# Kernel optimization log

Measured on AMD Instinct MI355X. Metric: run time of the kernel, lower is better.

Reference implementation:

```python
import jax, jax.numpy as jnp
import numpy as np

S, N, CIN, H, W = 8, 32, 128, 16, 16
COUT, K = 128, 3
F = CIN * K * K          # in_features = Cin*k*k = 1152
LAM = float(F)           # NealPrior: var = 1/fan_in -> precision = fan_in


def extract_patches(x):
    # x: [S,N,Cin,H,W] -> [S,N,F,H*W] patches, torch-unfold ordering (Cin outer, then ki,kj)
    p = K // 2
    xp = jnp.pad(x, ((0, 0), (0, 0), (0, 0), (p, p), (p, p)))
    pats = jnp.stack([xp[..., i:i + H, j:j + W] for i in range(K) for j in range(K)], axis=3)
    # pats: [S,N,Cin,K*K,H,W]
    return pats.reshape(x.shape[0], x.shape[1], F, H * W)


def setup_inputs() -> dict:
    key = jax.random.key(0)
    k1, k2, k3, k4 = jax.random.split(key, 4)
    X = jax.random.normal(k1, (S, N, CIN, H, W), jnp.float32)
    u = jax.random.normal(k2, (N, COUT, H, W), jnp.float32)
    log_prec_scaled = -4.0 + 0.1 * jax.random.normal(k3, (N,), jnp.float32)
    Z = jax.random.normal(k4, (S, F, COUT), jnp.float32)  # reparam noise (t.randn in torch fwd)
    return {"X": X, "u": u, "log_prec_scaled": log_prec_scaled, "Z": Z}


def reference(X, u, log_prec_scaled, Z):
    # sqrt per-inducing-point precision (log_prec_lr = 1.0)
    sqrt_prec = jnp.exp(0.5 * log_prec_scaled)
    Xil = sqrt_prec[None, :, None, None, None] * X       # [S,N,Cin,H,W]
    Yil = sqrt_prec[:, None, None, None] * u             # [N,Cout,H,W]

    Xu = extract_patches(Xil)                            # [S,N,F,L]
    Yr = Yil.reshape(N, COUT, H * W)                     # [N,Cout,L]

    XLX = jnp.einsum('snfl,sngl->sfg', Xu, Xu)           # [S,F,F]
    XLY = jnp.einsum('snfl,ncl->sfc', Xu, Yr)            # [S,F,Cout]

    prec = XLX + LAM * jnp.eye(F, dtype=X.dtype)         # add isotropic Neal prior precision
    L = jnp.linalg.cholesky(prec)                        # [S,F,F]
    logdet = 2.0 * jnp.sum(jnp.log(jnp.diagonal(L, axis1=-2, axis2=-1)), -1)  # [S]
    logdet_total = COUT * logdet                         # expand over out_features then sum

    # posterior mean: prec^{-1} XLY via two triangular solves (cholesky_solve)
    t1 = jax.scipy.linalg.solve_triangular(L, XLY, lower=True)
    mu = jax.scipy.linalg.solve_triangular(L, t1, lower=True, trans=1)
    # dW solves L^T dW = Z (triangular_solve upper=False, transpose=True)
    dW = jax.scipy.linalg.solve_triangular(L, Z, lower=True, trans=1)

    sample_fc = mu + dW                                  # [S,F,Cout]
    sample = jnp.swapaxes(sample_fc, -1, -2)             # [S,Cout,F] (torch layout)

    # logP: unnormalized MVN log-prob under isotropic Neal prior precision LAM
    logP = -0.5 * LAM * jnp.sum(sample_fc ** 2, (-1, -2)) \
           + 0.5 * COUT * F * jnp.log(jnp.asarray(LAM, X.dtype))
    logQ = -0.5 * jnp.sum(Z ** 2, (-1, -2)) + 0.5 * logdet_total
    logpq = logP - logQ                                  # [S]
    return sample, logpq
```

## Files before the change

### kernel.cpp

```cpp
#include <hip/hip_runtime.h>
#include <hip/hip_bf16.h>
#include <math.h>

#define NS    8
#define NNI   32
#define NCI   128
#define NHH   16
#define NWW   16
#define NCO   128
#define NFF   1152
#define NLL   256
#define LAMV  1152.0f
#define COOPG 512

typedef short s8v __attribute__((ext_vector_type(8)));
typedef float f4v __attribute__((ext_vector_type(4)));

#define AS1 __attribute__((address_space(1)))
#define AS3 __attribute__((address_space(3)))

__device__ __forceinline__ float rdl(float v, int l) {
  return __uint_as_float(__builtin_amdgcn_readlane(__float_as_uint(v), (unsigned)l));
}

#define WAVE_LDS_FENCE() asm volatile("s_waitcnt lgkmcnt(0)" ::: "memory")

__global__ __launch_bounds__(256) void k_build_Xu(const float* __restrict__ X,
                                                  const float* __restrict__ lp,
                                                  unsigned short* __restrict__ Xu,
                                                  int nz) {
  unsigned idx = blockIdx.x * 256u + threadIdx.x;
  unsigned m = idx & 8191u;
  unsigned f = idx >> 13;
  unsigned n = m >> 8, l = m & 255u, h = l >> 4, w = l & 15u;
  unsigned c = f / 9u, a = f - 9u * c;
  unsigned ki = a / 3u, kj = a - 3u * ki;
  int hi = (int)(h + ki) - 1, wi = (int)(w + kj) - 1;
  bool inb = (hi >= 0 && hi < NHH && wi >= 0 && wi < NWW);
  size_t xoff = (((size_t)n * NCI + c) << 8) + (size_t)(unsigned)(hi * NWW + wi);
  float spn = expf(0.5f * lp[n]);
  for (int z = 0; z < nz; ++z) {
    float v = inb ? X[(size_t)z * 1048576 + xoff] : 0.f;
    __hip_bfloat16 hv = __float2bfloat16(spn * v);
    Xu[(size_t)z * (NFF * 8192) + idx] = *(unsigned short*)&hv;
  }
}

__global__ __launch_bounds__(256) void k_build_B(const float* __restrict__ u,
                                                 const float* __restrict__ lp,
                                                 unsigned short* __restrict__ Bm) {
  unsigned idx = blockIdx.x * 256u + threadIdx.x;
  unsigned m = idx & 8191u;
  unsigned c = idx >> 13;
  unsigned n = m >> 8, l = m & 255u;
  float spn = expf(0.5f * lp[n]);
  __hip_bfloat16 hv = __float2bfloat16(spn * u[((size_t)n * NCO + c) * NLL + l]);
  Bm[idx] = *(unsigned short*)&hv;
}

__global__ void k_diag_init(float* __restrict__ prec) {
  int s = blockIdx.y;
  int i = blockIdx.x * 256 + threadIdx.x;
  if (i < NFF) prec[(size_t)s * NFF * NFF + (size_t)i * NFF + i] = LAMV;
}

__global__ __launch_bounds__(256) void k_mfma(const unsigned short* __restrict__ XuBase,
                                              const unsigned short* __restrict__ Bm,
                                              float* __restrict__ prec,
                                              float* __restrict__ XLY,
                                              int kLen, int direct) {
  __shared__ unsigned short As[8192];
  __shared__ unsigned short Bs[8192];
  int z = blockIdx.z;
  const unsigned short* Xu = XuBase + (size_t)z * (NFF * 8192);
  prec += (size_t)z * NFF * NFF;
  XLY += (size_t)z * NFF * NCO;
  int bx = blockIdx.x;
  int row0, col0;
  const unsigned short* Ag;
  const unsigned short* Bg;
  bool isXLX;
  if (bx < 45) {
    int b = 0;
    while ((b + 1) * (b + 2) / 2 <= bx) b++;
    row0 = b * 128;
    col0 = (bx - b * (b + 1) / 2) * 128;
    Bg = Xu + (size_t)col0 * 8192;
    isXLX = true;
  } else {
    row0 = (bx - 45) * 128;
    col0 = 0;
    Bg = Bm;
    isXLX = false;
  }
  Ag = Xu + (size_t)row0 * 8192;

  int t = threadIdx.x;
  int lane = t & 63, w = t >> 6;
  int wm = w & 1, wn = w >> 1;
  int n16 = lane & 15, q = lane >> 4;
  int srow = lane >> 3, sch = lane & 7;

  f4v acc[4][4];
#pragma unroll
  for (int i = 0; i < 4; ++i)
#pragma unroll
    for (int j = 0; j < 4; ++j) acc[i][j] = (f4v)0.f;

  int kBase = blockIdx.y * kLen;
  for (int k0 = kBase; k0 < kBase + kLen; k0 += 64) {
    __syncthreads();
#pragma unroll
    for (int it = 0; it < 4; ++it) {
      int rA = (w * 4 + it) * 8 + srow;
      int cA = (sch - rA) & 7;
      const unsigned short* gpa = Ag + (size_t)rA * 8192 + k0 + cA * 8;
      const unsigned short* gpb = Bg + (size_t)rA * 8192 + k0 + cA * 8;
      __builtin_amdgcn_global_load_lds((AS1 const void*)gpa,
                                       (AS3 void*)&As[(w * 4 + it) * 512], 16, 0, 0);
      __builtin_amdgcn_global_load_lds((AS1 const void*)gpb,
                                       (AS3 void*)&Bs[(w * 4 + it) * 512], 16, 0, 0);
    }
    __syncthreads();
#pragma unroll
    for (int kk = 0; kk < 2; ++kk) {
      s8v af[4], bf[4];
#pragma unroll
      for (int im = 0; im < 4; ++im) {
        int r = wm * 64 + im * 16 + n16;
        int slot = ((kk * 4 + q) + r) & 7;
        af[im] = *(const s8v*)&As[r * 64 + slot * 8];
      }
#pragma unroll
      for (int in = 0; in < 4; ++in) {
        int r = wn * 64 + in * 16 + n16;
        int slot = ((kk * 4 + q) + r) & 7;
        bf[in] = *(const s8v*)&Bs[r * 64 + slot * 8];
      }
#pragma unroll
      for (int im = 0; im < 4; ++im)
#pragma unroll
        for (int in = 0; in < 4; ++in)
          acc[im][in] = __builtin_amdgcn_mfma_f32_16x16x32_bf16(af[im], bf[in], acc[im][in], 0, 0, 0);
    }
  }

#pragma unroll
  for (int im = 0; im < 4; ++im)
#pragma unroll
    for (int in = 0; in < 4; ++in) {
      int gr = row0 + wm * 64 + im * 16 + q * 4;
      int gc = (isXLX ? col0 : 0) + wn * 64 + in * 16 + n16;
      if (direct) {
        if (isXLX) {
#pragma unroll
          for (int tt = 0; tt < 4; ++tt)
            prec[(size_t)(gr + tt) * NFF + gc] =
                acc[im][in][tt] + ((gr + tt) == gc ? LAMV : 0.f);
        } else {
#pragma unroll
          for (int tt = 0; tt < 4; ++tt)
            XLY[(size_t)(gr + tt) * NCO + gc] = acc[im][in][tt];
        }
      } else {
        if (isXLX) {
#pragma unroll
          for (int tt = 0; tt < 4; ++tt)
            atomicAdd(&prec[(size_t)(gr + tt) * NFF + gc], acc[im][in][tt]);
        } else {
#pragma unroll
          for (int tt = 0; tt < 4; ++tt)
            atomicAdd(&XLY[(size_t)(gr + tt) * NCO + gc], acc[im][in][tt]);
        }
      }
    }
}

__device__ __forceinline__ void xsync(unsigned* slot, unsigned* go, unsigned role,
                                      unsigned cnt, unsigned ep) {
  __syncthreads();
  int t = threadIdx.x;
  if (t == 0)
    __hip_atomic_store(&slot[role], ep, __ATOMIC_RELAXED, __HIP_MEMORY_SCOPE_AGENT);
  if (role == 0) {
    if (t < 64) {
      for (;;) {
        unsigned ok = 1;
        for (unsigned i = (unsigned)t; i < cnt; i += 64u)
          ok &= (__hip_atomic_load(&slot[i], __ATOMIC_RELAXED, __HIP_MEMORY_SCOPE_AGENT) >= ep)
                    ? 1u : 0u;
        if (__all((int)ok)) break;
        __builtin_amdgcn_s_sleep(2);
      }
      if (t == 0)
        __hip_atomic_store(go, ep, __ATOMIC_RELAXED, __HIP_MEMORY_SCOPE_AGENT);
    }
  } else if (t == 0) {
    while (__hip_atomic_load(go, __ATOMIC_RELAXED, __HIP_MEMORY_SCOPE_AGENT) < ep)
      __builtin_amdgcn_s_sleep(2);
  }
  __syncthreads();
  asm volatile("buffer_inv" ::: "memory");
  __syncthreads();
}

__device__ void dev_fact64(float* D, float* accum_ld, int lane) {
  float x[64];
#pragma unroll
  for (int k = 0; k < 64; ++k) x[k] = D[(size_t)lane * NFF + k];
  float ld = 0.f;
#pragma unroll
  for (int k = 0; k < 64; ++k) {
    float dk = sqrtf(rdl(x[k], k));
    float inv = 1.0f / dk;
    ld += logf(dk);
    x[k] = (lane == k) ? dk : ((lane > k) ? x[k] * inv : x[k]);
#pragma unroll
    for (int kk = k + 1; kk < 64; ++kk)
      x[kk] = fmaf(-x[k], rdl(x[k], kk), x[kk]);
  }
  if (lane == 0) atomicAdd(accum_ld, 2.f * ld);
#pragma unroll
  for (int k = 0; k < 64; ++k) D[(size_t)lane * NFF + k] = x[k];
}

__device__ void dev_panel(float* Ps, int p, int i, float* smw) {
  float (*Xs)[66] = (float(*)[66])smw;
  const float* Dp = Ps + (size_t)(p * 64) * NFF + p * 64;
  float* Ai = Ps + (size_t)(i * 64) * NFF + p * 64;
  float* At = Ps + (size_t)(p * 64) * NFF + i * 64;
  int lane = threadIdx.x & 63;
  float Lc[64];
#pragma unroll
  for (int k = 0; k < 64; ++k) Lc[k] = Dp[(size_t)k * NFF + lane];
  for (int r = 0; r < 64; ++r) Xs[r][lane] = Ai[(size_t)r * NFF + lane];
  WAVE_LDS_FENCE();
  float x[64];
#pragma unroll
  for (int k = 0; k < 64; ++k) x[k] = Xs[lane][k];
#pragma unroll
  for (int j = 0; j < 64; ++j) {
    float xj = x[j] / rdl(Lc[j], j);
    x[j] = xj;
#pragma unroll
    for (int k = j + 1; k < 64; ++k)
      x[k] = fmaf(-xj, rdl(Lc[k], j), x[k]);
  }
#pragma unroll
  for (int k = 0; k < 64; ++k) Xs[lane][k] = x[k];
  WAVE_LDS_FENCE();
  for (int r = 0; r < 64; ++r) At[(size_t)r * NFF + lane] = Xs[lane][r];
}

__device__ void dev_trail(float* Ps, float* accum, int p, int idx, float* sm) {
  int b = 0;
  while ((b + 1) * (b + 2) / 2 <= idx) b++;
  int c = idx - b * (b + 1) / 2;
  int i = p + 1 + b, j = p + 1 + c;
  const float* Ui = Ps + (size_t)(p * 64) * NFF + i * 64;
  const float* Uj = Ps + (size_t)(p * 64) * NFF + j * 64;
  float* Cb = Ps + (size_t)(i * 64) * NFF + j * 64;
  float (*Ak)[68] = (float(*)[68])sm;
  float (*Bk)[68] = (float(*)[68])(sm + 4352);
  int t = threadIdx.x, tx = t & 15, ty = t >> 4;
  __syncthreads();
  for (int e = t; e < 1024; e += 256) {
    int k = e >> 4, c4 = (e & 15) * 4;
    *(float4*)&Ak[k][c4] = *(const float4*)(Ui + (size_t)k * NFF + c4);
    *(float4*)&Bk[k][c4] = *(const float4*)(Uj + (size_t)k * NFF + c4);
  }
  __syncthreads();
  float acc[4][4];
#pragma unroll
  for (int a = 0; a < 4; ++a)
#pragma unroll
    for (int b2 = 0; b2 < 4; ++b2) acc[a][b2] = 0.f;
#pragma unroll
  for (int kk = 0; kk < 64; ++kk) {
    float av[4], bv[4];
    *(float4*)&av[0] = *(const float4*)&Ak[kk][ty * 4];
    *(float4*)&bv[0] = *(const float4*)&Bk[kk][tx * 4];
#pragma unroll
    for (int a = 0; a < 4; ++a)
#pragma unroll
      for (int b2 = 0; b2 < 4; ++b2) acc[a][b2] = fmaf(av[a], bv[b2], acc[a][b2]);
  }
  if (!(b == 0 && c == 0)) {
#pragma unroll
    for (int a = 0; a < 4; ++a) {
      float4* cp = (float4*)(Cb + (size_t)(ty * 4 + a) * NFF + tx * 4);
      float4 cv = *cp;
      cv.x -= acc[a][0]; cv.y -= acc[a][1]; cv.z -= acc[a][2]; cv.w -= acc[a][3];
      *cp = cv;
    }
  } else {
    __syncthreads();
#pragma unroll
    for (int a = 0; a < 4; ++a) {
      float4 cv = *(const float4*)(Cb + (size_t)(ty * 4 + a) * NFF + tx * 4);
      cv.x -= acc[a][0]; cv.y -= acc[a][1]; cv.z -= acc[a][2]; cv.w -= acc[a][3];
      *(float4*)&Ak[ty * 4 + a][tx * 4] = cv;
    }
    __syncthreads();
    if (t < 64) {
      int lane = t;
      float x[64];
#pragma unroll
      for (int k = 0; k < 64; ++k) x[k] = Ak[lane][k];
      float ld = 0.f;
#pragma unroll
      for (int k = 0; k < 64; ++k) {
        float dk = sqrtf(rdl(x[k], k));
        float inv = 1.0f / dk;
        ld += logf(dk);
        x[k] = (lane == k) ? dk : ((lane > k) ? x[k] * inv : x[k]);
#pragma unroll
        for (int kk = k + 1; kk < 64; ++kk)
          x[kk] = fmaf(-x[k], rdl(x[k], kk), x[kk]);
      }
      if (lane == 0) atomicAdd(accum, 2.f * ld);
#pragma unroll
      for (int k = 0; k < 64; ++k) Ak[lane][k] = x[k];
    }
    __syncthreads();
    for (int e = t; e < 1024; e += 256) {
      int r = e >> 4, c4 = (e & 15) * 4;
      *(float4*)(Cb + (size_t)r * NFF + c4) = *(float4*)&Ak[r][c4];
    }
  }
}

__device__ void dev_invdiag(const float* Ps, float* Ws, int lane) {
  float Lr[64];
#pragma unroll
  for (int m = 0; m < 64; ++m) Lr[m] = Ps[(size_t)lane * NFF + m];
  float x[64];
#pragma unroll
  for (int k = 0; k < 64; ++k) {
    float v = (lane == k) ? 1.f : 0.f;
#pragma unroll
    for (int m = 0; m < k; ++m)
      v = fmaf(-rdl(Lr[m], k), x[m], v);
    x[k] = v / rdl(Lr[k], k);
  }
#pragma unroll
  for (int k = 0; k < 64; ++k) Ws[(size_t)k * NFF + lane] = x[k];
}

__device__ void dev_inv1(const float* Ps, float* Ws, int p, float* sm) {
  int J = 2 * p, I = 2 * p + 1;
  float (*Ak)[65] = (float(*)[65])sm;
  float (*Bk)[65] = (float(*)[65])(sm + 4160);
  float (*Dk)[65] = (float(*)[65])(sm + 8320);
  float (*Tt)[65] = (float(*)[65])(sm + 12480);
  int t = threadIdx.x, tx = t & 15, ty = t >> 4;
  __syncthreads();
  for (int e = t; e < 4096; e += 256) {
    int r = e >> 6, cc = e & 63;
    Ak[r][cc] = Ps[(size_t)(J * 64 + r) * NFF + I * 64 + cc];
    Bk[r][cc] = Ws[(size_t)(J * 64 + r) * NFF + J * 64 + cc];
  }
  {
    int i = t >> 2;
#pragma unroll
    for (int it = 0; it < 4; ++it) {
      int kq = (t & 3) * 4 + it * 16;
      float4 a = *(const float4*)&Ws[(size_t)(I * 64 + i) * NFF + I * 64 + kq];
      Dk[kq + 0][i] = a.x; Dk[kq + 1][i] = a.y; Dk[kq + 2][i] = a.z; Dk[kq + 3][i] = a.w;
    }
  }
  __syncthreads();
  float acc[4][4];
#pragma unroll
  for (int a = 0; a < 4; ++a)
#pragma unroll
    for (int b = 0; b < 4; ++b) acc[a][b] = 0.f;
#pragma unroll 8
  for (int kk = 0; kk < 64; ++kk) {
    float av[4], bv[4];
#pragma unroll
    for (int a = 0; a < 4; ++a) av[a] = Ak[kk][ty * 4 + a];
#pragma unroll
    for (int b = 0; b < 4; ++b) bv[b] = Bk[kk][tx * 4 + b];
#pragma unroll
    for (int a = 0; a < 4; ++a)
#pragma unroll
      for (int b = 0; b < 4; ++b) acc[a][b] = fmaf(av[a], bv[b], acc[a][b]);
  }
#pragma unroll
  for (int a = 0; a < 4; ++a)
#pragma unroll
    for (int b = 0; b < 4; ++b) Tt[ty * 4 + a][tx * 4 + b] = acc[a][b];
  __syncthreads();
  float a2[4][4];
#pragma unroll
  for (int a = 0; a < 4; ++a)
#pragma unroll
    for (int b = 0; b < 4; ++b) a2[a][b] = 0.f;
#pragma unroll 8
  for (int kk = 0; kk < 64; ++kk) {
    float av[4], bv[4];
#pragma unroll
    for (int a = 0; a < 4; ++a) av[a] = Dk[kk][ty * 4 + a];
#pragma unroll
    for (int b = 0; b < 4; ++b) bv[b] = Tt[kk][tx * 4 + b];
#pragma unroll
    for (int a = 0; a < 4; ++a)
#pragma unroll
      for (int b = 0; b < 4; ++b) a2[a][b] = fmaf(av[a], bv[b], a2[a][b]);
  }
#pragma unroll
  for (int a = 0; a < 4; ++a) {
    float4 o;
    o.x = -a2[a][0]; o.y = -a2[a][1]; o.z = -a2[a][2]; o.w = -a2[a][3];
    *(float4*)&Ws[(size_t)(I * 64 + ty * 4 + a) * NFF + J * 64 + tx * 4] = o;
  }
}

__device__ void dev_invA(const float* Ps, const float* Ws, float* Tbs,
                         int n1, int n2, int nc, int c0, int r, int ccb, int pq,
                         float* sm) {
  int ldT = nc * 64;
  int o = pq * 2 * n1;
  int I = o + n1 + r, c = c0 + ccb;
  float* Ts = Tbs + (size_t)pq * (size_t)(n2 * 64) * ldT;
  float (*Aks)[68] = (float(*)[68])sm;
  float (*Bks)[68] = (float(*)[68])(sm + 1088);
  int t = threadIdx.x, tx = t & 15, ty = t >> 4;
  float acc[4][4];
#pragma unroll
  for (int a = 0; a < 4; ++a)
#pragma unroll
    for (int b = 0; b < 4; ++b) acc[a][b] = 0.f;
  for (int kb = c; kb < n1; ++kb) {
    const float* up = Ps + (size_t)((o + kb) * 64) * NFF + I * 64;
    const float* wp = Ws + (size_t)((o + kb) * 64) * NFF + (o + c) * 64;
    for (int k0 = 0; k0 < 64; k0 += 16) {
      float4 a = *(const float4*)(up + (size_t)(k0 + ty) * NFF + tx * 4);
      float4 b = *(const float4*)(wp + (size_t)(k0 + ty) * NFF + tx * 4);
      __syncthreads();
      *(float4*)&Aks[ty][tx * 4] = a;
      *(float4*)&Bks[ty][tx * 4] = b;
      __syncthreads();
#pragma unroll
      for (int kk = 0; kk < 16; ++kk) {
        float av[4], bv[4];
        *(float4*)&av[0] = *(const float4*)&Aks[kk][ty * 4];
        *(float4*)&bv[0] = *(const float4*)&Bks[kk][tx * 4];
#pragma unroll
        for (int a2 = 0; a2 < 4; ++a2)
#pragma unroll
          for (int b2 = 0; b2 < 4; ++b2) acc[a2][b2] = fmaf(av[a2], bv[b2], acc[a2][b2]);
      }
    }
  }
#pragma unroll
  for (int a = 0; a < 4; ++a) {
    float4 v;
    v.x = acc[a][0]; v.y = acc[a][1]; v.z = acc[a][2]; v.w = acc[a][3];
    *(float4*)(Ts + (size_t)(r * 64 + ty * 4 + a) * ldT + ccb * 64 + tx * 4) = v;
  }
}

__device__ void dev_invB(float* Ws, const float* Tbs,
                         int n1, int n2, int nc, int c0, int r, int ccb, int pq,
                         float* sm) {
  int ldT = nc * 64;
  int o = pq * 2 * n1;
  int I = o + n1 + r, c = c0 + ccb;
  const float* Ts = Tbs + (size_t)pq * (size_t)(n2 * 64) * ldT;
  float (*Aks)[68] = (float(*)[68])sm;
  float (*Bks)[68] = (float(*)[68])(sm + 1088);
  int t = threadIdx.x, tx = t & 15, ty = t >> 4;
  float acc[4][4];
#pragma unroll
  for (int a = 0; a < 4; ++a)
#pragma unroll
    for (int b = 0; b < 4; ++b) acc[a][b] = 0.f;
  for (int kb = 0; kb <= r; ++kb) {
    const float* ap = Ws + (size_t)(I * 64) * NFF + (o + n1 + kb) * 64;
    const float* tp = Ts + (size_t)(kb * 64) * ldT + ccb * 64;
    for (int k0 = 0; k0 < 64; k0 += 16) {
      float4 a = *(const float4*)(ap + (size_t)(t >> 2) * NFF + k0 + (t & 3) * 4);
      float4 b = *(const float4*)(tp + (size_t)(k0 + ty) * ldT + tx * 4);
      __syncthreads();
      Aks[(t & 3) * 4 + 0][t >> 2] = a.x;
      Aks[(t & 3) * 4 + 1][t >> 2] = a.y;
      Aks[(t & 3) * 4 + 2][t >> 2] = a.z;
      Aks[(t & 3) * 4 + 3][t >> 2] = a.w;
      *(float4*)&Bks[ty][tx * 4] = b;
      __syncthreads();
#pragma unroll
      for (int kk = 0; kk < 16; ++kk) {
        float av[4], bv[4];
        *(float4*)&av[0] = *(const float4*)&Aks[kk][ty * 4];
        *(float4*)&bv[0] = *(const float4*)&Bks[kk][tx * 4];
#pragma unroll
        for (int a2 = 0; a2 < 4; ++a2)
#pragma unroll
          for (int b2 = 0; b2 < 4; ++b2) acc[a2][b2] = fmaf(av[a2], bv[b2], acc[a2][b2]);
      }
    }
  }
#pragma unroll
  for (int a = 0; a < 4; ++a) {
    float4 v;
    v.x = -acc[a][0]; v.y = -acc[a][1]; v.z = -acc[a][2]; v.w = -acc[a][3];
    *(float4*)&Ws[(size_t)(I * 64 + ty * 4 + a) * NFF + (o + c) * 64 + tx * 4] = v;
  }
}

__device__ void dev_app1(const float* Ws, const float* Ys, const float* Zs,
                         float* Os, float* accum, int rb, int ch, int s, float* sm) {
  int r0 = rb * 64, c0 = ch * 64;
  float (*As_)[68] = (float(*)[68])sm;
  float (*Bs_)[68] = (float(*)[68])(sm + 1088);
  float* red = sm + 2176;
  int t = threadIdx.x, tx = t & 15, ty = t >> 4;
  float acc[4][4];
#pragma unroll
  for (int a = 0; a < 4; ++a)
#pragma unroll
    for (int b = 0; b < 4; ++b) acc[a][b] = 0.f;
  int kmax = r0 + 64;
  for (int k0 = 0; k0 < kmax; k0 += 16) {
    float4 a = *(const float4*)(Ws + (size_t)(r0 + (t >> 2)) * NFF + k0 + (t & 3) * 4);
    float4 bb = *(const float4*)(Ys + (size_t)(k0 + (t >> 4)) * NCO + c0 + (t & 15) * 4);
    __syncthreads();
    As_[(t & 3) * 4 + 0][t >> 2] = a.x; As_[(t & 3) * 4 + 1][t >> 2] = a.y;
    As_[(t & 3) * 4 + 2][t >> 2] = a.z; As_[(t & 3) * 4 + 3][t >> 2] = a.w;
    *(float4*)&Bs_[t >> 4][(t & 15) * 4] = bb;
    __syncthreads();
#pragma unroll
    for (int kk = 0; kk < 16; ++kk) {
      float av[4], bv[4];
      *(float4*)&av[0] = *(const float4*)&As_[kk][ty * 4];
      *(float4*)&bv[0] = *(const float4*)&Bs_[kk][tx * 4];
#pragma unroll
      for (int a2 = 0; a2 < 4; ++a2)
#pragma unroll
        for (int b2 = 0; b2 < 4; ++b2) acc[a2][b2] = fmaf(av[a2], bv[b2], acc[a2][b2]);
    }
  }
  float z2 = 0.f;
#pragma unroll
  for (int a2 = 0; a2 < 4; ++a2) {
    int row = r0 + ty * 4 + a2;
    const float* zp = Zs + (size_t)row * NCO + c0 + tx * 4;
    float* op = Os + (size_t)row * NCO + c0 + tx * 4;
    float4 z0 = *(const float4*)zp;
    float4 v0;
    v0.x = acc[a2][0] + z0.x; v0.y = acc[a2][1] + z0.y;
    v0.z = acc[a2][2] + z0.z; v0.w = acc[a2][3] + z0.w;
    z2 += z0.x * z0.x + z0.y * z0.y + z0.z * z0.z + z0.w * z0.w;
    *(float4*)op = v0;
  }
  __syncthreads();
  red[t] = z2;
  __syncthreads();
  for (int o = 128; o > 0; o >>= 1) {
    if (t < o) red[t] += red[t + o];
    __syncthreads();
  }
  if (t == 0) atomicAdd(&accum[s * 4 + 1], red[0]);
}

__device__ void dev_app2(const float* Ws, const float* Rs, float* Op,
                         float* accum, int rb, int ch, int s, float* sm) {
  int r0 = rb * 64, c0 = ch * 64;
  float (*As_)[68] = (float(*)[68])sm;
  float (*Bs_)[68] = (float(*)[68])(sm + 1088);
  float* red = sm + 2176;
  int t = threadIdx.x, tx = t & 15, ty = t >> 4;
  float acc[4][4];
#pragma unroll
  for (int a = 0; a < 4; ++a)
#pragma unroll
    for (int b = 0; b < 4; ++b) acc[a][b] = 0.f;
  for (int k0 = r0; k0 < NFF; k0 += 16) {
    float4 a = *(const float4*)(Ws + (size_t)(k0 + (t >> 4)) * NFF + r0 + (t & 15) * 4);
    float4 bb = *(const float4*)(Rs + (size_t)(k0 + (t >> 4)) * NCO + c0 + (t & 15) * 4);
    __syncthreads();
    *(float4*)&As_[t >> 4][(t & 15) * 4] = a;
    *(float4*)&Bs_[t >> 4][(t & 15) * 4] = bb;
    __syncthreads();
#pragma unroll
    for (int kk = 0; kk < 16; ++kk) {
      float av[4], bv[4];
      *(float4*)&av[0] = *(const float4*)&As_[kk][ty * 4];
      *(float4*)&bv[0] = *(const float4*)&Bs_[kk][tx * 4];
#pragma unroll
      for (int a2 = 0; a2 < 4; ++a2)
#pragma unroll
        for (int b2 = 0; b2 < 4; ++b2) acc[a2][b2] = fmaf(av[a2], bv[b2], acc[a2][b2]);
    }
  }
  float s2 = 0.f;
#pragma unroll
  for (int b2 = 0; b2 < 4; ++b2) {
    int col = c0 + tx * 4 + b2;
    float4 v;
    v.x = acc[0][b2]; v.y = acc[1][b2]; v.z = acc[2][b2]; v.w = acc[3][b2];
    s2 += v.x * v.x + v.y * v.y + v.z * v.z + v.w * v.w;
    *(float4*)(Op + (size_t)col * NFF + r0 + ty * 4) = v;
  }
  __syncthreads();
  red[t] = s2;
  __syncthreads();
  for (int o = 128; o > 0; o >>= 1) {
    if (t < o) red[t] += red[t + o];
    __syncthreads();
  }
  if (t == 0) atomicAdd(&accum[s * 4 + 0], red[0]);
}

__global__ __launch_bounds__(256, 2) void k_coop(float* __restrict__ prec,
                                                 float* __restrict__ W,
                                                 const float* __restrict__ XLY,
                                                 float* __restrict__ t1R,
                                                 const float* __restrict__ Z,
                                                 float* __restrict__ out,
                                                 float* __restrict__ accum,
                                                 unsigned* __restrict__ syncmem) {
  __shared__ float SM[16896];
  __shared__ unsigned shr[2];
  int t = threadIdx.x;
  int wv = t >> 6, lane = t & 63;

  unsigned xcd;
  asm("s_getreg_b32 %0, hwreg(HW_REG_XCC_ID)" : "=s"(xcd));
  xcd &= 7u;
  unsigned* regcnt = syncmem;
  unsigned* garr = syncmem + 8;
  unsigned* go = syncmem + 64 + xcd * 16;
  unsigned* slot = syncmem + 256 + xcd * 512;
  if (t == 0) {
    unsigned r = __hip_atomic_fetch_add(&regcnt[xcd], 1u,
                                        __ATOMIC_RELAXED, __HIP_MEMORY_SCOPE_AGENT);
    asm volatile("s_waitcnt vmcnt(0)" ::: "memory");
    __hip_atomic_fetch_add(garr, 1u, __ATOMIC_RELAXED, __HIP_MEMORY_SCOPE_AGENT);
    while (__hip_atomic_load(garr, __ATOMIC_RELAXED, __HIP_MEMORY_SCOPE_AGENT) < gridDim.x)
      __builtin_amdgcn_s_sleep(8);
    shr[0] = r;
    shr[1] = __hip_atomic_load(&regcnt[xcd], __ATOMIC_RELAXED, __HIP_MEMORY_SCOPE_AGENT);
  }
  __syncthreads();
  unsigned role = shr[0], cnt = shr[1];

  int s = (int)xcd;
  float* Ps = prec + (size_t)s * NFF * NFF;
  float* Wsb = W + (size_t)s * NFF * NFF;
  const float* Ys = XLY + (size_t)s * 147456;
  float* Rs = t1R + (size_t)s * 147456;
  const float* Zs = Z + (size_t)s * 147456;
  float* Outp = out + (size_t)s * 147456;
  unsigned ep = 0;
#define GS() xsync(slot, go, role, cnt, ++ep)

  if (role == 0 && wv == 0) dev_fact64(Ps, &accum[s * 4 + 2], lane);
  GS();

  for (int p = 0; p < 17; ++p) {
    int m = 17 - p;
    for (unsigned tau = role * 4 + wv; tau < (unsigned)m; tau += cnt * 4)
      dev_panel(Ps, p, p + 1 + (int)tau, SM + wv * 4224);
    GS();
    unsigned nt = (unsigned)(m * (m + 1) / 2);
    for (unsigned tau = role; tau < nt; tau += cnt)
      dev_trail(Ps, &accum[s * 4 + 2], p, (int)tau, SM);
    GS();
  }

  for (unsigned tau = role * 4 + wv; tau < 18u; tau += cnt * 4) {
    const float* Pd = Ps + (size_t)(tau * 64) * NFF + tau * 64;
    float* Wd = Wsb + (size_t)(tau * 64) * NFF + tau * 64;
    dev_invdiag(Pd, Wd, lane);
  }
  GS();

  for (unsigned tau = role; tau < 9u; tau += cnt)
    dev_inv1(Ps, Wsb, (int)tau, SM);
  GS();

  {
    const int LV[5][4] = { {2, 2, 2, 0}, {4, 4, 4, 0},
                           {8, 8, 4, 0}, {8, 8, 4, 4}, {16, 2, 16, 0} };
    const int NP[5] = {4, 2, 1, 1, 1};
    for (int lv = 0; lv < 5; ++lv) {
      int n1 = LV[lv][0], n2 = LV[lv][1], nc = LV[lv][2], c0 = LV[lv][3], np = NP[lv];
      unsigned ntask = (unsigned)(n2 * nc * np);
      for (unsigned tau = role; tau < ntask; tau += cnt) {
        unsigned q = tau;
        int r = (int)(q % (unsigned)n2); q /= (unsigned)n2;
        int ccb = (int)(q % (unsigned)nc); int pq = (int)(q / (unsigned)nc);
        dev_invA(Ps, Wsb, Rs, n1, n2, nc, c0, r, ccb, pq, SM);
      }
      GS();
      for (unsigned tau = role; tau < ntask; tau += cnt) {
        unsigned q = tau;
        int r = (int)(q % (unsigned)n2); q /= (unsigned)n2;
        int ccb = (int)(q % (unsigned)nc); int pq = (int)(q / (unsigned)nc);
        dev_invB(Wsb, Rs, n1, n2, nc, c0, r, ccb, pq, SM);
      }
      GS();
    }
  }

  for (unsigned tau = role; tau < 36u; tau += cnt) {
    int ch = (int)(tau & 1u), rb = (int)(tau >> 1);
    dev_app1(Wsb, Ys, Zs, Rs, accum, rb, ch, s, SM);
  }
  GS();
  for (unsigned tau = role; tau < 36u; tau += cnt) {
    int ch = (int)(tau & 1u), rb = (int)(tau >> 1);
    dev_app2(Wsb, Rs, Outp, accum, rb, ch, s, SM);
  }
  GS();
  if (role == 0 && t == 0) {
    float s2 = __hip_atomic_load(&accum[s * 4 + 0], __ATOMIC_RELAXED, __HIP_MEMORY_SCOPE_AGENT);
    float z2 = __hip_atomic_load(&accum[s * 4 + 1], __ATOMIC_RELAXED, __HIP_MEMORY_SCOPE_AGENT);
    float ld = __hip_atomic_load(&accum[s * 4 + 2], __ATOMIC_RELAXED, __HIP_MEMORY_SCOPE_AGENT);
    float logP = -0.5f * LAMV * s2 + 0.5f * (float)(NCO * NFF) * logf(LAMV);
    float logQ = -0.5f * z2 + 0.5f * (float)NCO * ld;
    out[(size_t)NS * 147456 + s] = logP - logQ;
  }
#undef GS
}

extern "C" void kernel_launch(void* const* d_in, const int* in_sizes, int n_in,
                              void* d_out, int out_size, void* d_ws, size_t ws_size,
                              hipStream_t stream) {
  const float* X = (const float*)d_in[0];
  const float* u = (const float*)d_in[1];
  const float* lp = (const float*)d_in[2];
  const float* Z = (const float*)d_in[3];
  float* out = (float*)d_out;

  const size_t XU2 = 18874368;
  const size_t BM2 = 2097152;
  const size_t FF4 = 5308416;
  const size_t FC4 = 589824;
  const size_t FC = 147456;
  const size_t FF = 1327104;
  const size_t XSTR = 1048576;

  int SB, kslices;
  if (ws_size >= ((size_t)206 << 20))      { SB = 8; kslices = 1; }
  else if (ws_size >= ((size_t)131 << 20)) { SB = 4; kslices = 2; }
  else                                     { SB = 2; kslices = 4; }

  char* ws = (char*)d_ws;
  size_t reg0 = (size_t)SB * XU2 + BM2;
  if (reg0 < 8 * FF4) reg0 = 8 * FF4;
  unsigned short* Xu = (unsigned short*)ws;
  unsigned short* Bm = (unsigned short*)(ws + (size_t)SB * XU2);
  float* W = (float*)ws;
  size_t off = reg0;
  float* prec = (float*)(ws + off); off += 8 * FF4;
  float* XLY = (float*)(ws + off);  off += 8 * FC4;
  float* t1R = (float*)(ws + off);  off += 8 * FC4;
  float* accum = (float*)(ws + off);
  unsigned* syncmem = (unsigned*)(ws + off + 512);

  k_build_B<<<4096, 256, 0, stream>>>(u, lp, Bm);
  hipMemsetAsync(accum, 0, 512 + 20480, stream);
  if (kslices > 1) {
    hipMemsetAsync(prec, 0, 8 * FF4, stream);
    hipMemsetAsync(XLY, 0, 8 * FC4, stream);
    k_diag_init<<<dim3(5, 8), 256, 0, stream>>>(prec);
  }

  for (int pr = 0; pr < 8 / SB; ++pr) {
    k_build_Xu<<<36864, 256, 0, stream>>>(X + (size_t)pr * SB * XSTR, lp, Xu, SB);
    k_mfma<<<dim3(54, kslices, SB), 256, 0, stream>>>(Xu, Bm,
                                                      prec + (size_t)pr * SB * FF,
                                                      XLY + (size_t)pr * SB * FC,
                                                      8192 / kslices, kslices == 1 ? 1 : 0);
  }

  k_coop<<<COOPG, 256, 0, stream>>>(prec, W, XLY, t1R, Z, out, accum, syncmem);
}
```

Before: 1.741 ms.

## Keep owned Cholesky tiles resident in LDS across the blocked factorization

Each workgroup statically owns up to three 64x64 lower-triangle tiles of the precision matrix and keeps them in LDS for the whole blocked Cholesky. Trailing updates subtract into the LDS copy instead of reading and writing global memory, and panel solves and diagonal factorizations read from LDS. The diagonal factorization is also fused into the trailing step, which removes the separate 'diagonal tile' branch. Trail GEMM operands now stream in 16-row chunks through a small shared buffer. This cuts global traffic and cache-coherence pressure per step, at the cost of more LDS per block and a global fallback path (with buffer_inv) when fewer than 57 roles exist.

After: 1.709 ms. Within noise of the previous version (-1.9%).

```diff
diff --git a/kernel.cpp b/kernel.cpp
--- a/kernel.cpp
+++ b/kernel.cpp
@@ -22,8 +22,6 @@
 __device__ __forceinline__ float rdl(float v, int l) {
   return __uint_as_float(__builtin_amdgcn_readlane(__float_as_uint(v), (unsigned)l));
 }
-
-#define WAVE_LDS_FENCE() asm volatile("s_waitcnt lgkmcnt(0)" ::: "memory")
 
 __global__ __launch_bounds__(256) void k_build_Xu(const float* __restrict__ X,
                                                   const float* __restrict__ lp,
@@ -224,20 +222,33 @@
   for (int k = 0; k < 64; ++k) D[(size_t)lane * NFF + k] = x[k];
 }
 
-__device__ void dev_panel(float* Ps, int p, int i, float* smw) {
-  float (*Xs)[66] = (float(*)[66])smw;
-  const float* Dp = Ps + (size_t)(p * 64) * NFF + p * 64;
-  float* Ai = Ps + (size_t)(i * 64) * NFF + p * 64;
-  float* At = Ps + (size_t)(p * 64) * NFF + i * 64;
-  int lane = threadIdx.x & 63;
+__device__ void dev_factLds(const float* T68, float* Dg, float* accum_ld, int lane) {
+  float x[64];
+#pragma unroll
+  for (int k = 0; k < 64; ++k) x[k] = T68[lane * 68 + k];
+  float ld = 0.f;
+#pragma unroll
+  for (int k = 0; k < 64; ++k) {
+    float dk = sqrtf(rdl(x[k], k));
+    float inv = 1.0f / dk;
+    ld += logf(dk);
+    x[k] = (lane == k) ? dk : ((lane > k) ? x[k] * inv : x[k]);
+#pragma unroll
+    for (int kk = k + 1; kk < 64; ++kk)
+      x[kk] = fmaf(-x[k], rdl(x[k], kk), x[kk]);
+  }
+  if (lane == 0) atomicAdd(accum_ld, 2.f * ld);
+#pragma unroll
+  for (int k = 0; k < 64; ++k) Dg[(size_t)lane * NFF + k] = x[k];
+}
+
+__device__ void dev_panelLds(const float* T68, const float* Dg, float* At, int lane) {
   float Lc[64];
 #pragma unroll
-  for (int k = 0; k < 64; ++k) Lc[k] = Dp[(size_t)k * NFF + lane];
-  for (int r = 0; r < 64; ++r) Xs[r][lane] = Ai[(size_t)r * NFF + lane];
-  WAVE_LDS_FENCE();
+  for (int k = 0; k < 64; ++k) Lc[k] = Dg[(size_t)k * NFF + lane];
   float x[64];
 #pragma unroll
-  for (int k = 0; k < 64; ++k) x[k] = Xs[lane][k];
+  for (int k = 0; k < 64; ++k) x[k] = T68[lane * 68 + k];
 #pragma unroll
   for (int j = 0; j < 64; ++j) {
     float xj = x[j] / rdl(Lc[j], j);
@@ -247,85 +258,73 @@
       x[k] = fmaf(-xj, rdl(Lc[k], j), x[k]);
   }
 #pragma unroll
-  for (int k = 0; k < 64; ++k) Xs[lane][k] = x[k];
-  WAVE_LDS_FENCE();
-  for (int r = 0; r < 64; ++r) At[(size_t)r * NFF + lane] = Xs[lane][r];
-}
-
-__device__ void dev_trail(float* Ps, float* accum, int p, int idx, float* sm) {
-  int b = 0;
-  while ((b + 1) * (b + 2) / 2 <= idx) b++;
-  int c = idx - b * (b + 1) / 2;
-  int i = p + 1 + b, j = p + 1 + c;
+  for (int r = 0; r < 64; ++r) At[(size_t)r * NFF + lane] = x[r];
+}
+
+__device__ void dev_panelGlb(const float* AiG, const float* Dg, float* At, int lane) {
+  float Lc[64];
+#pragma unroll
+  for (int k = 0; k < 64; ++k) Lc[k] = Dg[(size_t)k * NFF + lane];
+  float x[64];
+#pragma unroll
+  for (int k = 0; k < 64; ++k) x[k] = AiG[(size_t)lane * NFF + k];
+#pragma unroll
+  for (int j = 0; j < 64; ++j) {
+    float xj = x[j] / rdl(Lc[j], j);
+    x[j] = xj;
+#pragma unroll
+    for (int k = j + 1; k < 64; ++k)
+      x[k] = fmaf(-xj, rdl(Lc[k], j), x[k]);
+  }
+#pragma unroll
+  for (int r = 0; r < 64; ++r) At[(size_t)r * NFF + lane] = x[r];
+}
+
+__device__ void dev_trail2(float* Ps, float* tileT, int p, int i, int j, float* csm) {
   const float* Ui = Ps + (size_t)(p * 64) * NFF + i * 64;
   const float* Uj = Ps + (size_t)(p * 64) * NFF + j * 64;
-  float* Cb = Ps + (size_t)(i * 64) * NFF + j * 64;
-  float (*Ak)[68] = (float(*)[68])sm;
-  float (*Bk)[68] = (float(*)[68])(sm + 4352);
+  float (*Ak)[68] = (float(*)[68])csm;
+  float (*Bk)[68] = (float(*)[68])(csm + 1088);
   int t = threadIdx.x, tx = t & 15, ty = t >> 4;
-  __syncthreads();
-  for (int e = t; e < 1024; e += 256) {
-    int k = e >> 4, c4 = (e & 15) * 4;
-    *(float4*)&Ak[k][c4] = *(const float4*)(Ui + (size_t)k * NFF + c4);
-    *(float4*)&Bk[k][c4] = *(const float4*)(Uj + (size_t)k * NFF + c4);
-  }
-  __syncthreads();
   float acc[4][4];
 #pragma unroll
   for (int a = 0; a < 4; ++a)
 #pragma unroll
     for (int b2 = 0; b2 < 4; ++b2) acc[a][b2] = 0.f;
-#pragma unroll
-  for (int kk = 0; kk < 64; ++kk) {
-    float av[4], bv[4];
-    *(float4*)&av[0] = *(const float4*)&Ak[kk][ty * 4];
-    *(float4*)&bv[0] = *(const float4*)&Bk[kk][tx * 4];
-#pragma unroll
-    for (int a = 0; a < 4; ++a)
-#pragma unroll
-      for (int b2 = 0; b2 < 4; ++b2) acc[a][b2] = fmaf(av[a], bv[b2], acc[a][b2]);
-  }
-  if (!(b == 0 && c == 0)) {
+  for (int k0 = 0; k0 < 64; k0 += 16) {
+    float4 a = *(const float4*)(Ui + (size_t)(k0 + ty) * NFF + tx * 4);
+    float4 b = *(const float4*)(Uj + (size_t)(k0 + ty) * NFF + tx * 4);
+    __syncthreads();
+    *(float4*)&Ak[ty][tx * 4] = a;
+    *(float4*)&Bk[ty][tx * 4] = b;
+    __syncthreads();
+#pragma unroll
+    for (int kk = 0; kk < 16; ++kk) {
+      float av[4], bv[4];
+      *(float4*)&av[0] = *(const float4*)&Ak[kk][ty * 4];
+      *(float4*)&bv[0] = *(const float4*)&Bk[kk][tx * 4];
+#pragma unroll
+      for (int a2 = 0; a2 < 4; ++a2)
+#pragma unroll
+        for (int b2 = 0; b2 < 4; ++b2) acc[a2][b2] = fmaf(av[a2], bv[b2], acc[a2][b2]);
+    }
+  }
+  if (tileT) {
+#pragma unroll
+    for (int a = 0; a < 4; ++a) {
+      float4* cp = (float4*)&tileT[(ty * 4 + a) * 68 + tx * 4];
+      float4 cv = *cp;
+      cv.x -= acc[a][0]; cv.y -= acc[a][1]; cv.z -= acc[a][2]; cv.w -= acc[a][3];
+      *cp = cv;
+    }
+  } else {
+    float* Cb = Ps + (size_t)(i * 64) * NFF + j * 64;
 #pragma unroll
     for (int a = 0; a < 4; ++a) {
       float4* cp = (float4*)(Cb + (size_t)(ty * 4 + a) * NFF + tx * 4);
       float4 cv = *cp;
       cv.x -= acc[a][0]; cv.y -= acc[a][1]; cv.z -= acc[a][2]; cv.w -= acc[a][3];
       *cp = cv;
-    }
-  } else {
-    __syncthreads();
-#pragma unroll
-    for (int a = 0; a < 4; ++a) {
-      float4 cv = *(const float4*)(Cb + (size_t)(ty * 4 + a) * NFF + tx * 4);
-      cv.x -= acc[a][0]; cv.y -= acc[a][1]; cv.z -= acc[a][2]; cv.w -= acc[a][3];
-      *(float4*)&Ak[ty * 4 + a][tx * 4] = cv;
-    }
-    __syncthreads();
-    if (t < 64) {
-      int lane = t;
-      float x[64];
-#pragma unroll
-      for (int k = 0; k < 64; ++k) x[k] = Ak[lane][k];
-      float ld = 0.f;
-#pragma unroll
-      for (int k = 0; k < 64; ++k) {
-        float dk = sqrtf(rdl(x[k], k));
-        float inv = 1.0f / dk;
-        ld += logf(dk);
-        x[k] = (lane == k) ? dk : ((lane > k) ? x[k] * inv : x[k]);
-#pragma unroll
-        for (int kk = k + 1; kk < 64; ++kk)
-          x[kk] = fmaf(-x[k], rdl(x[k], kk), x[kk]);
-      }
-      if (lane == 0) atomicAdd(accum, 2.f * ld);
-#pragma unroll
-      for (int k = 0; k < 64; ++k) Ak[lane][k] = x[k];
-    }
-    __syncthreads();
-    for (int e = t; e < 1024; e += 256) {
-      int r = e >> 4, c4 = (e & 15) * 4;
-      *(float4*)(Cb + (size_t)r * NFF + c4) = *(float4*)&Ak[r][c4];
     }
   }
 }
@@ -647,27 +646,96 @@
   __syncthreads();
   unsigned role = shr[0], cnt = shr[1];
 
-  int s = (int)xcd;
-  float* Ps = prec + (size_t)s * NFF * NFF;
-  float* Wsb = W + (size_t)s * NFF * NFF;
-  const float* Ys = XLY + (size_t)s * 147456;
-  float* Rs = t1R + (size_t)s * 147456;
-  const float* Zs = Z + (size_t)s * 147456;
-  float* Outp = out + (size_t)s * 147456;
+  int smp = (int)xcd;
+  float* Ps = prec + (size_t)smp * NFF * NFF;
+  float* Wsb = W + (size_t)smp * NFF * NFF;
+  const float* Ys = XLY + (size_t)smp * 147456;
+  float* Rs = t1R + (size_t)smp * 147456;
+  const float* Zs = Z + (size_t)smp * 147456;
+  float* Outp = out + (size_t)smp * 147456;
   unsigned ep = 0;
 #define GS() xsync(slot, go, role, cnt, ++ep)
 
-  if (role == 0 && wv == 0) dev_fact64(Ps, &accum[s * 4 + 2], lane);
+  int ti[3], tj[3];
+  bool tv[3];
+#pragma unroll
+  for (int sl = 0; sl < 3; ++sl) {
+    unsigned tt = role + (unsigned)sl * cnt;
+    tv[sl] = (tt < 171u);
+    ti[sl] = 0; tj[sl] = 0;
+    if (tv[sl]) {
+      int i = 0;
+      while ((unsigned)((i + 1) * (i + 2) / 2) <= tt) ++i;
+      ti[sl] = i;
+      tj[sl] = (int)tt - i * (i + 1) / 2;
+    }
+  }
+
+#pragma unroll
+  for (int sl = 0; sl < 3; ++sl)
+    if (tv[sl]) {
+      const float* Gb = Ps + (size_t)(ti[sl] * 64) * NFF + tj[sl] * 64;
+      float* T = SM + sl * 4352;
+      for (int e = t; e < 1024; e += 256) {
+        int r = e >> 4, c4 = (e & 15) * 4;
+        *(float4*)&T[r * 68 + c4] = *(const float4*)(Gb + (size_t)r * NFF + c4);
+      }
+    }
+  __syncthreads();
+
+  if (role == 0 && t < 64) dev_factLds(SM, Ps, &accum[smp * 4 + 2], t);
   GS();
 
   for (int p = 0; p < 17; ++p) {
-    int m = 17 - p;
-    for (unsigned tau = role * 4 + wv; tau < (unsigned)m; tau += cnt * 4)
-      dev_panel(Ps, p, p + 1 + (int)tau, SM + wv * 4224);
+#pragma unroll
+    for (int sl = 0; sl < 3; ++sl)
+      if (wv == sl && tv[sl] && tj[sl] == p && ti[sl] > p)
+        dev_panelLds(SM + sl * 4352, Ps + (size_t)(p * 64) * NFF + p * 64,
+                     Ps + (size_t)(p * 64) * NFF + ti[sl] * 64, lane);
+    if (cnt < 57u && wv == 3) {
+      for (unsigned tt = role + 3u * cnt; tt < 171u; tt += cnt) {
+        int i = 0;
+        while ((unsigned)((i + 1) * (i + 2) / 2) <= tt) ++i;
+        int j = (int)tt - i * (i + 1) / 2;
+        if (j == p && i > p)
+          dev_panelGlb(Ps + (size_t)(i * 64) * NFF + p * 64,
+                       Ps + (size_t)(p * 64) * NFF + p * 64,
+                       Ps + (size_t)(p * 64) * NFF + i * 64, lane);
+      }
+    }
     GS();
-    unsigned nt = (unsigned)(m * (m + 1) / 2);
-    for (unsigned tau = role; tau < nt; tau += cnt)
-      dev_trail(Ps, &accum[s * 4 + 2], p, (int)tau, SM);
+#pragma unroll
+    for (int sl = 0; sl < 3; ++sl)
+      if (tv[sl] && ti[sl] > p && tj[sl] > p)
+        dev_trail2(Ps, SM + sl * 4352, p, ti[sl], tj[sl], SM + 13056);
+    if (cnt < 57u) {
+      for (unsigned tt = role + 3u * cnt; tt < 171u; tt += cnt) {
+        int i = 0;
+        while ((unsigned)((i + 1) * (i + 2) / 2) <= tt) ++i;
+        int j = (int)tt - i * (i + 1) / 2;
+        if (i > p && j > p) dev_trail2(Ps, nullptr, p, i, j, SM + 13056);
+      }
+    }
+    {
+      int dn = p + 1;
+#pragma unroll
+      for (int sl = 0; sl < 3; ++sl)
+        if (tv[sl] && ti[sl] == dn && tj[sl] == dn) {
+          __syncthreads();
+          if (t < 64)
+            dev_factLds(SM + sl * 4352, Ps + (size_t)(dn * 64) * NFF + dn * 64,
+                        &accum[smp * 4 + 2], t);
+        }
+      if (cnt < 57u) {
+        unsigned td = (unsigned)(dn * (dn + 1) / 2 + dn);
+        if (td % cnt == role && td / cnt >= 3u) {
+          __syncthreads();
+          asm volatile("buffer_inv" ::: "memory");
+          if (t < 64)
+            dev_fact64(Ps + (size_t)(dn * 64) * NFF + dn * 64, &accum[smp * 4 + 2], t);
+        }
+      }
+    }
     GS();
   }
 
@@ -708,21 +776,21 @@
 
   for (unsigned tau = role; tau < 36u; tau += cnt) {
     int ch = (int)(tau & 1u), rb = (int)(tau >> 1);
-    dev_app1(Wsb, Ys, Zs, Rs, accum, rb, ch, s, SM);
+    dev_app1(Wsb, Ys, Zs, Rs, accum, rb, ch, smp, SM);
   }
   GS();
   for (unsigned tau = role; tau < 36u; tau += cnt) {
     int ch = (int)(tau & 1u), rb = (int)(tau >> 1);
-    dev_app2(Wsb, Rs, Outp, accum, rb, ch, s, SM);
+    dev_app2(Wsb, Rs, Outp, accum, rb, ch, smp, SM);
   }
   GS();
   if (role == 0 && t == 0) {
-    float s2 = __hip_atomic_load(&accum[s * 4 + 0], __ATOMIC_RELAXED, __HIP_MEMORY_SCOPE_AGENT);
-    float z2 = __hip_atomic_load(&accum[s * 4 + 1], __ATOMIC_RELAXED, __HIP_MEMORY_SCOPE_AGENT);
-    float ld = __hip_atomic_load(&accum[s * 4 + 2], __ATOMIC_RELAXED, __HIP_MEMORY_SCOPE_AGENT);
+    float s2 = __hip_atomic_load(&accum[smp * 4 + 0], __ATOMIC_RELAXED, __HIP_MEMORY_SCOPE_AGENT);
+    float z2 = __hip_atomic_load(&accum[smp * 4 + 1], __ATOMIC_RELAXED, __HIP_MEMORY_SCOPE_AGENT);
+    float ld = __hip_atomic_load(&accum[smp * 4 + 2], __ATOMIC_RELAXED, __HIP_MEMORY_SCOPE_AGENT);
     float logP = -0.5f * LAMV * s2 + 0.5f * (float)(NCO * NFF) * logf(LAMV);
     float logQ = -0.5f * z2 + 0.5f * (float)NCO * ld;
-    out[(size_t)NS * 147456 + s] = logP - logQ;
+    out[(size_t)NS * 147456 + smp] = logP - logQ;
   }
 #undef GS
 }
```
